# Kernel optimization log

Hardware: AMD Instinct MI355X
Metric: run time of the kernel (lower is better)

The kernel has to match this reference:

```python
import jax, jax.numpy as jnp
import numpy as np

D_INNER = 512; D_STATE = 16; DT_RANK = 32; D_CONV = 4; NUM_NODES = 32
B_ = 4; T_ = 128; F_IN = 64; F_OUT = 64


def setup_inputs() -> dict:
    key = jax.random.key(0)
    ks = jax.random.split(key, 8)
    s = 0.02
    x = jax.random.normal(ks[0], (B_, NUM_NODES, T_, F_IN), jnp.float32)
    adj_matrix = jax.random.randint(ks[1], (NUM_NODES, NUM_NODES), 0, 2, jnp.int32)
    W_in = jax.random.normal(ks[2], (F_IN, 2 * D_INNER), jnp.float32) * s
    W_conv = jax.random.normal(ks[3], (D_INNER, 1, D_CONV), jnp.float32) * s  # depthwise (O,I/g,K)
    b_conv = jnp.zeros((D_INNER,), jnp.float32)
    W_xproj = jax.random.normal(ks[4], (D_INNER, DT_RANK + 2 * D_STATE), jnp.float32) * s
    W_dt = jax.random.normal(ks[5], (DT_RANK, D_INNER), jnp.float32) * s
    b_dt = jnp.zeros((D_INNER,), jnp.float32)
    A_log = jnp.log(jnp.broadcast_to(jnp.arange(1, D_STATE + 1, dtype=jnp.float32), (D_INNER, D_STATE)))
    D = jnp.ones((D_INNER,), jnp.float32)
    W_out = jax.random.normal(ks[6], (D_INNER, F_OUT), jnp.float32) * s
    return dict(x=x, adj_matrix=adj_matrix, W_in=W_in, W_conv=W_conv, b_conv=b_conv,
                W_xproj=W_xproj, W_dt=W_dt, b_dt=b_dt, A_log=A_log, D=D, W_out=W_out)


def reference(x, adj_matrix, W_in, W_conv, b_conv, W_xproj, W_dt, b_dt, A_log, D, W_out):
    b, n_nodes, t, f = x.shape
    u0 = x.reshape(b * n_nodes, t, f)                     # (B, l, f)
    xz = u0 @ W_in                                        # (B, l, 2*d_inner)
    xc, res = jnp.split(xz, 2, axis=-1)
    # causal depthwise conv1d (torch: pad=k-1 both sides then truncate == left-pad k-1)
    xt = jnp.transpose(xc, (0, 2, 1))                     # (B, d, l)
    xt = jnp.pad(xt, ((0, 0), (0, 0), (D_CONV - 1, 0)))
    xt = jax.lax.conv_general_dilated(xt, W_conv, (1,), 'VALID',
        dimension_numbers=('NCH', 'OIH', 'NCH'), feature_group_count=D_INNER)
    xt = xt + b_conv[None, :, None]
    u = jax.nn.silu(jnp.transpose(xt, (0, 2, 1)))         # (B, l, d)
    # SSM parameterization
    A = -jnp.exp(A_log)                                   # (d, n)
    x_dbl = u @ W_xproj
    dlt, Bm, Cm = jnp.split(x_dbl, [DT_RANK, DT_RANK + D_STATE], axis=-1)
    delta = jax.nn.softplus(dlt @ W_dt + b_dt)            # (B, l, d)
    # adjacency padded into ones(d_inner, d_inner) top-left corner
    pad = jnp.ones((D_INNER, D_INNER), jnp.float32)
    pad = pad.at[:NUM_NODES, :NUM_NODES].set(adj_matrix.astype(jnp.float32))
    delta_p = delta @ pad                                 # (B, l, d)
    deltaA = jnp.exp(jnp.einsum('bld,dn->bldn', delta_p, A))
    deltaBu = jnp.einsum('bld,bln->bldn', delta_p * u, Bm)

    def step(h, inp):
        dA_t, dBu_t, C_t = inp
        h = dA_t * h + dBu_t                              # (B, d, n)
        y = jnp.einsum('bdn,bn->bd', h, C_t)
        return h, y

    h0 = jnp.zeros((b * n_nodes, D_INNER, D_STATE), jnp.float32)
    _, ys = jax.lax.scan(step, h0,
        (jnp.moveaxis(deltaA, 1, 0), jnp.moveaxis(deltaBu, 1, 0), jnp.moveaxis(Cm, 1, 0)))
    y = jnp.moveaxis(ys, 0, 1)                            # (B, l, d)
    # original detaches recurrence state and y each step -> scan output carries no grad
    y = jax.lax.stop_gradient(y) + u * D
    y = y * jax.nn.silu(res)
    return y @ W_out                                      # (B, l, dim_out)
```

## Files before the change

### kernel.cpp

```cpp
#include <hip/hip_runtime.h>
#include <cmath>

#define T_    128
#define F_    64
#define DI    512
#define DS    16
#define NROW  16384

#define U_OFF    0u
#define SRES_OFF 8388608u
#define DPH_OFF  16777216u
#define DPT_OFF  17301504u
#define B_OFF    17317888u
#define C_OFF    17580032u

__device__ __forceinline__ float silu_f(float v)    { return v / (1.f + __expf(-v)); }
__device__ __forceinline__ float softplus_f(float v){ return (v > 20.f) ? v : log1pf(__expf(v)); }

__global__ __launch_bounds__(256) void k1_inproj(
    const float* __restrict__ x, const float* __restrict__ W_in,
    const float* __restrict__ W_conv, const float* __restrict__ b_conv,
    float* __restrict__ u, float* __restrict__ sres)
{
    __shared__ float x_l[19][64];
    const int s  = blockIdx.y;
    const int t0 = blockIdx.x * 16;
    const int c4 = threadIdx.x * 4;

    for (int i = threadIdx.x; i < 19 * 16; i += 256) {
        const int row = i >> 4, col = (i & 15) * 4;
        const int trow = t0 - 3 + row;
        float4 v = make_float4(0.f, 0.f, 0.f, 0.f);
        if (trow >= 0) v = *(const float4*)&x[(size_t)s * (T_ * F_) + trow * F_ + col];
        *(float4*)&x_l[row][col] = v;
    }
    __syncthreads();

    float4 acc[19];
#pragma unroll
    for (int i = 0; i < 19; ++i) acc[i] = make_float4(0.f, 0.f, 0.f, 0.f);

    for (int f0 = 0; f0 < F_; f0 += 8) {
        float4 wv[8];
#pragma unroll
        for (int j = 0; j < 8; ++j)
            wv[j] = *(const float4*)&W_in[(size_t)(f0 + j) * 1024 + c4];
#pragma unroll
        for (int tt = 0; tt < 19; ++tt) {
            const float4 xa = *(const float4*)&x_l[tt][f0];
            const float4 xb = *(const float4*)&x_l[tt][f0 + 4];
            float4 a = acc[tt];
            a.x = fmaf(xa.x, wv[0].x, a.x); a.y = fmaf(xa.x, wv[0].y, a.y);
            a.z = fmaf(xa.x, wv[0].z, a.z); a.w = fmaf(xa.x, wv[0].w, a.w);
            a.x = fmaf(xa.y, wv[1].x, a.x); a.y = fmaf(xa.y, wv[1].y, a.y);
            a.z = fmaf(xa.y, wv[1].z, a.z); a.w = fmaf(xa.y, wv[1].w, a.w);
            a.x = fmaf(xa.z, wv[2].x, a.x); a.y = fmaf(xa.z, wv[2].y, a.y);
            a.z = fmaf(xa.z, wv[2].z, a.z); a.w = fmaf(xa.z, wv[2].w, a.w);
            a.x = fmaf(xa.w, wv[3].x, a.x); a.y = fmaf(xa.w, wv[3].y, a.y);
            a.z = fmaf(xa.w, wv[3].z, a.z); a.w = fmaf(xa.w, wv[3].w, a.w);
            a.x = fmaf(xb.x, wv[4].x, a.x); a.y = fmaf(xb.x, wv[4].y, a.y);
            a.z = fmaf(xb.x, wv[4].z, a.z); a.w = fmaf(xb.x, wv[4].w, a.w);
            a.x = fmaf(xb.y, wv[5].x, a.x); a.y = fmaf(xb.y, wv[5].y, a.y);
            a.z = fmaf(xb.y, wv[5].z, a.z); a.w = fmaf(xb.y, wv[5].w, a.w);
            a.x = fmaf(xb.z, wv[6].x, a.x); a.y = fmaf(xb.z, wv[6].y, a.y);
            a.z = fmaf(xb.z, wv[6].z, a.z); a.w = fmaf(xb.z, wv[6].w, a.w);
            a.x = fmaf(xb.w, wv[7].x, a.x); a.y = fmaf(xb.w, wv[7].y, a.y);
            a.z = fmaf(xb.w, wv[7].z, a.z); a.w = fmaf(xb.w, wv[7].w, a.w);
            acc[tt] = a;
        }
    }

    if (c4 < DI) {
        const float4 wk0 = *(const float4*)&W_conv[(c4 + 0) * 4];
        const float4 wk1 = *(const float4*)&W_conv[(c4 + 1) * 4];
        const float4 wk2 = *(const float4*)&W_conv[(c4 + 2) * 4];
        const float4 wk3 = *(const float4*)&W_conv[(c4 + 3) * 4];
        const float4 bc  = *(const float4*)&b_conv[c4];
#pragma unroll
        for (int i = 0; i < 16; ++i) {
            float4 pre;
            pre.x = bc.x; pre.y = bc.y; pre.z = bc.z; pre.w = bc.w;
            pre.x = fmaf(wk0.x, acc[i].x, pre.x); pre.x = fmaf(wk0.y, acc[i+1].x, pre.x);
            pre.x = fmaf(wk0.z, acc[i+2].x, pre.x); pre.x = fmaf(wk0.w, acc[i+3].x, pre.x);
            pre.y = fmaf(wk1.x, acc[i].y, pre.y); pre.y = fmaf(wk1.y, acc[i+1].y, pre.y);
            pre.y = fmaf(wk1.z, acc[i+2].y, pre.y); pre.y = fmaf(wk1.w, acc[i+3].y, pre.y);
            pre.z = fmaf(wk2.x, acc[i].z, pre.z); pre.z = fmaf(wk2.y, acc[i+1].z, pre.z);
            pre.z = fmaf(wk2.z, acc[i+2].z, pre.z); pre.z = fmaf(wk2.w, acc[i+3].z, pre.z);
            pre.w = fmaf(wk3.x, acc[i].w, pre.w); pre.w = fmaf(wk3.y, acc[i+1].w, pre.w);
            pre.w = fmaf(wk3.z, acc[i+2].w, pre.w); pre.w = fmaf(wk3.w, acc[i+3].w, pre.w);
            float4 o;
            o.x = silu_f(pre.x); o.y = silu_f(pre.y);
            o.z = silu_f(pre.z); o.w = silu_f(pre.w);
            *(float4*)&u[(size_t)(s * T_ + t0 + i) * DI + c4] = o;
        }
    } else {
        const int c = c4 - DI;
#pragma unroll
        for (int i = 0; i < 16; ++i) {
            float4 o;
            o.x = silu_f(acc[i + 3].x); o.y = silu_f(acc[i + 3].y);
            o.z = silu_f(acc[i + 3].z); o.w = silu_f(acc[i + 3].w);
            *(float4*)&sres[(size_t)(s * T_ + t0 + i) * DI + c] = o;
        }
    }
}

__global__ __launch_bounds__(256) void k2a_xproj(
    const float* __restrict__ uin, const float* __restrict__ W_xp,
    float* __restrict__ dlt, float* __restrict__ Bb, float* __restrict__ Cb)
{
    __shared__ float y_l[64][68];
    __shared__ float w_l[64][64];
    const int tid = threadIdx.x;
    const int rq = tid >> 4, cq = tid & 15;
    const int r0 = blockIdx.x * 64;
    const int c4 = cq * 4;

    float4 acc[4];
#pragma unroll
    for (int i = 0; i < 4; ++i) acc[i] = make_float4(0.f, 0.f, 0.f, 0.f);

    for (int kc = 0; kc < DI; kc += 64) {
        for (int i = tid; i < 64 * 16; i += 256) {
            const int row = i >> 4, cc = (i & 15) * 4;
            *(float4*)&y_l[row][cc] = *(const float4*)&uin[(size_t)(r0 + row) * DI + kc + cc];
            *(float4*)&w_l[row][cc] = *(const float4*)&W_xp[(size_t)(kc + row) * 64 + cc];
        }
        __syncthreads();
#pragma unroll 4
        for (int kk = 0; kk < 64; kk += 4) {
            float4 yv[4], wv[4];
#pragma unroll
            for (int i = 0; i < 4; ++i) yv[i] = *(const float4*)&y_l[rq * 4 + i][kk];
#pragma unroll
            for (int j = 0; j < 4; ++j) wv[j] = *(const float4*)&w_l[kk + j][c4];
#pragma unroll
            for (int i = 0; i < 4; ++i) {
                float4 a = acc[i];
                a.x = fmaf(yv[i].x, wv[0].x, a.x); a.y = fmaf(yv[i].x, wv[0].y, a.y);
                a.z = fmaf(yv[i].x, wv[0].z, a.z); a.w = fmaf(yv[i].x, wv[0].w, a.w);
                a.x = fmaf(yv[i].y, wv[1].x, a.x); a.y = fmaf(yv[i].y, wv[1].y, a.y);
                a.z = fmaf(yv[i].y, wv[1].z, a.z); a.w = fmaf(yv[i].y, wv[1].w, a.w);
                a.x = fmaf(yv[i].z, wv[2].x, a.x); a.y = fmaf(yv[i].z, wv[2].y, a.y);
                a.z = fmaf(yv[i].z, wv[2].z, a.z); a.w = fmaf(yv[i].z, wv[2].w, a.w);
                a.x = fmaf(yv[i].w, wv[3].x, a.x); a.y = fmaf(yv[i].w, wv[3].y, a.y);
                a.z = fmaf(yv[i].w, wv[3].z, a.z); a.w = fmaf(yv[i].w, wv[3].w, a.w);
                acc[i] = a;
            }
        }
        __syncthreads();
    }
#pragma unroll
    for (int i = 0; i < 4; ++i) {
        const int r = r0 + rq * 4 + i;
        if (c4 < 32)      *(float4*)&dlt[(size_t)r * 32 + c4]        = acc[i];
        else if (c4 < 48) *(float4*)&Bb [(size_t)r * DS + (c4 - 32)] = acc[i];
        else              *(float4*)&Cb [(size_t)r * DS + (c4 - 48)] = acc[i];
    }
}

__global__ __launch_bounds__(256) void k2b_delta(
    const float* __restrict__ dlt_in, const float* __restrict__ W_dt,
    const float* __restrict__ b_dt, const int* __restrict__ adj,
    float* __restrict__ dph, float* __restrict__ dpt)
{
    __shared__ float dl_l[32][32];
    __shared__ float head_l[32][33];
    __shared__ float scrS[4][32];
    __shared__ float stail_l[32];
    __shared__ float adj_l[1024];

    const int tid  = threadIdx.x;
    const int lane = tid & 63, wv4 = tid >> 6;
    const int r0   = blockIdx.x * 32;

    {
        const int row = tid >> 3, cc = (tid & 7) * 4;
        *(float4*)&dl_l[row][cc] = *(const float4*)&dlt_in[(size_t)(r0 + row) * 32 + cc];
        for (int i = tid; i < 1024; i += 256) adj_l[i] = (float)adj[i];
    }

    float wdt0[32], wdt1[32];
#pragma unroll
    for (int j = 0; j < 32; ++j) {
        wdt0[j] = W_dt[j * DI + tid];
        wdt1[j] = W_dt[j * DI + tid + 256];
    }
    const float b0 = b_dt[tid], b1 = b_dt[tid + 256];
    __syncthreads();

    for (int r = 0; r < 32; ++r) {
        float a0 = b0, a1 = b1;
#pragma unroll
        for (int jq = 0; jq < 8; ++jq) {
            const float4 dv = *(const float4*)&dl_l[r][jq * 4];
            a0 = fmaf(dv.x, wdt0[jq*4+0], a0); a1 = fmaf(dv.x, wdt1[jq*4+0], a1);
            a0 = fmaf(dv.y, wdt0[jq*4+1], a0); a1 = fmaf(dv.y, wdt1[jq*4+1], a1);
            a0 = fmaf(dv.z, wdt0[jq*4+2], a0); a1 = fmaf(dv.z, wdt1[jq*4+2], a1);
            a0 = fmaf(dv.w, wdt0[jq*4+3], a0); a1 = fmaf(dv.w, wdt1[jq*4+3], a1);
        }
        const float e0 = softplus_f(a0), e1 = softplus_f(a1);
        if (tid < 32) head_l[r][tid] = e0;
        float v = e0 + e1;
#pragma unroll
        for (int off = 32; off > 0; off >>= 1) v += __shfl_down(v, off, 64);
        if (lane == 0) scrS[wv4][r] = v;
    }
    __syncthreads();
    if (tid < 32) {
        const int r = tid;
        const float st = scrS[0][r] + scrS[1][r] + scrS[2][r] + scrS[3][r];
        dpt[r0 + r] = st;
        float sh = 0.f;
#pragma unroll
        for (int j = 0; j < 32; ++j) sh += head_l[r][j];
        stail_l[r] = st - sh;
    }
    __syncthreads();
#pragma unroll
    for (int k = 0; k < 4; ++k) {
        const int o = k * 256 + tid;
        const int r = o >> 5, dd = o & 31;
        float a = stail_l[r];
#pragma unroll
        for (int j = 0; j < 32; ++j) a = fmaf(head_l[r][j], adj_l[j * 32 + dd], a);
        dph[(size_t)(r0 + r) * 32 + dd] = a;
    }
}

__global__ __launch_bounds__(256) void k3_scan(
    const float* __restrict__ u, float* __restrict__ sres_y,
    const float* __restrict__ dph, const float* __restrict__ dpt,
    const float* __restrict__ Bb, const float* __restrict__ Cb,
    const float* __restrict__ A_log, const float* __restrict__ Dvec)
{
    const int s = blockIdx.y;
    const int d = blockIdx.x * 256 + threadIdx.x;
    float A[DS];
#pragma unroll
    for (int n = 0; n < DS; ++n) A[n] = -__expf(A_log[d * DS + n]);
    const float Dd = Dvec[d];
    const bool isHead = (d < 32);

    const size_t rb = (size_t)s * T_;
    const float* up   = u      + rb * DI + d;
    float*       gp   = sres_y + rb * DI + d;
    const float* dphp = dph + rb * 32 + d;
    const float* dptp = dpt + rb;
    const float4* Bp  = (const float4*)(Bb + rb * DS);
    const float4* Cp  = (const float4*)(Cb + rb * DS);

    float h[DS];
#pragma unroll
    for (int n = 0; n < DS; ++n) h[n] = 0.f;

    float ub[4], gb[4], dpb[4];
#pragma unroll
    for (int j = 0; j < 4; ++j) {
        ub[j]  = up[(size_t)j * DI];
        gb[j]  = gp[(size_t)j * DI];
        dpb[j] = isHead ? dphp[(size_t)j * 32] : dptp[j];
    }
    float4 bB[2][4], bC[2][4];
#pragma unroll
    for (int j = 0; j < 2; ++j)
#pragma unroll
        for (int q = 0; q < 4; ++q) { bB[j][q] = Bp[j * 4 + q]; bC[j][q] = Cp[j * 4 + q]; }

    for (int t = 0; t < T_; t += 4) {
#pragma unroll
        for (int j = 0; j < 4; ++j) {
            const int tc = t + j;
            const float u_c = ub[j], g_c = gb[j], dp_c = dpb[j];
            const float du = dp_c * u_c;
            float y0 = 0.f, y1 = 0.f, y2 = 0.f, y3 = 0.f;
#pragma unroll
            for (int q = 0; q < 4; ++q) {
                const float4 Bv = bB[j & 1][q];
                const float4 Cv = bC[j & 1][q];
                const int n = q * 4;
                const float e0 = __expf(dp_c * A[n + 0]);
                const float e1 = __expf(dp_c * A[n + 1]);
                const float e2 = __expf(dp_c * A[n + 2]);
                const float e3 = __expf(dp_c * A[n + 3]);
                h[n + 0] = fmaf(e0, h[n + 0], du * Bv.x);
                h[n + 1] = fmaf(e1, h[n + 1], du * Bv.y);
                h[n + 2] = fmaf(e2, h[n + 2], du * Bv.z);
                h[n + 3] = fmaf(e3, h[n + 3], du * Bv.w);
                y0 = fmaf(h[n + 0], Cv.x, y0);
                y1 = fmaf(h[n + 1], Cv.y, y1);
                y2 = fmaf(h[n + 2], Cv.z, y2);
                y3 = fmaf(h[n + 3], Cv.w, y3);
            }
            const float yf = (((y0 + y1) + (y2 + y3)) + u_c * Dd) * g_c;
            gp[(size_t)tc * DI] = yf;
            if (tc + 4 < T_) {
                ub[j]  = up[(size_t)(tc + 4) * DI];
                gb[j]  = gp[(size_t)(tc + 4) * DI];
                dpb[j] = isHead ? dphp[(size_t)(tc + 4) * 32] : dptp[tc + 4];
            }
            if (tc + 2 < T_) {
#pragma unroll
                for (int q = 0; q < 4; ++q) {
                    bB[j & 1][q] = Bp[(tc + 2) * 4 + q];
                    bC[j & 1][q] = Cp[(tc + 2) * 4 + q];
                }
            }
        }
    }
}

__global__ __launch_bounds__(256) void k4_out(
    const float* __restrict__ y, const float* __restrict__ W_out,
    float* __restrict__ out)
{
    __shared__ float y_l[64][68];
    __shared__ float w_l[64][64];
    const int tid = threadIdx.x;
    const int rq = tid >> 4, cq = tid & 15;
    const int r0 = blockIdx.x * 64;
    const int c4 = cq * 4;

    float4 acc[4];
#pragma unroll
    for (int i = 0; i < 4; ++i) acc[i] = make_float4(0.f, 0.f, 0.f, 0.f);

    for (int kc = 0; kc < DI; kc += 64) {
        for (int i = tid; i < 64 * 16; i += 256) {
            const int row = i >> 4, cc = (i & 15) * 4;
            *(float4*)&y_l[row][cc] = *(const float4*)&y[(size_t)(r0 + row) * DI + kc + cc];
            *(float4*)&w_l[row][cc] = *(const float4*)&W_out[(size_t)(kc + row) * 64 + cc];
        }
        __syncthreads();
#pragma unroll 4
        for (int kk = 0; kk < 64; kk += 4) {
            float4 yv[4], wv[4];
#pragma unroll
            for (int i = 0; i < 4; ++i) yv[i] = *(const float4*)&y_l[rq * 4 + i][kk];
#pragma unroll
            for (int j = 0; j < 4; ++j) wv[j] = *(const float4*)&w_l[kk + j][c4];
#pragma unroll
            for (int i = 0; i < 4; ++i) {
                float4 a = acc[i];
                a.x = fmaf(yv[i].x, wv[0].x, a.x); a.y = fmaf(yv[i].x, wv[0].y, a.y);
                a.z = fmaf(yv[i].x, wv[0].z, a.z); a.w = fmaf(yv[i].x, wv[0].w, a.w);
                a.x = fmaf(yv[i].y, wv[1].x, a.x); a.y = fmaf(yv[i].y, wv[1].y, a.y);
                a.z = fmaf(yv[i].y, wv[1].z, a.z); a.w = fmaf(yv[i].y, wv[1].w, a.w);
                a.x = fmaf(yv[i].z, wv[2].x, a.x); a.y = fmaf(yv[i].z, wv[2].y, a.y);
                a.z = fmaf(yv[i].z, wv[2].z, a.z); a.w = fmaf(yv[i].z, wv[2].w, a.w);
                a.x = fmaf(yv[i].w, wv[3].x, a.x); a.y = fmaf(yv[i].w, wv[3].y, a.y);
                a.z = fmaf(yv[i].w, wv[3].z, a.z); a.w = fmaf(yv[i].w, wv[3].w, a.w);
                acc[i] = a;
            }
        }
        __syncthreads();
    }
#pragma unroll
    for (int i = 0; i < 4; ++i)
        *(float4*)&out[(size_t)(r0 + rq * 4 + i) * 64 + c4] = acc[i];
}

extern "C" void kernel_launch(void* const* d_in, const int* in_sizes, int n_in,
                              void* d_out, int out_size, void* d_ws, size_t ws_size,
                              hipStream_t stream)
{
    const float* x      = (const float*)d_in[0];
    const int*   adj    = (const int*)  d_in[1];
    const float* W_in   = (const float*)d_in[2];
    const float* W_conv = (const float*)d_in[3];
    const float* b_conv = (const float*)d_in[4];
    const float* W_xp   = (const float*)d_in[5];
    const float* W_dt   = (const float*)d_in[6];
    const float* b_dt   = (const float*)d_in[7];
    const float* A_log  = (const float*)d_in[8];
    const float* Dvec   = (const float*)d_in[9];
    const float* W_out  = (const float*)d_in[10];

    float* ws   = (float*)d_ws;
    float* u    = ws + U_OFF;
    float* sres = ws + SRES_OFF;
    float* dB   = ws + DPH_OFF;
    float* dpt  = ws + DPT_OFF;
    float* Bb   = ws + B_OFF;
    float* Cb   = ws + C_OFF;
    float* out  = (float*)d_out;

    k1_inproj<<<dim3(8, 128), 256, 0, stream>>>(x, W_in, W_conv, b_conv, u, sres);
    k2a_xproj<<<dim3(256),    256, 0, stream>>>(u, W_xp, dB, Bb, Cb);
    k2b_delta<<<dim3(512),    256, 0, stream>>>(dB, W_dt, b_dt, adj, dB, dpt);
    k3_scan  <<<dim3(2, 128), 256, 0, stream>>>(u, sres, dB, dpt, Bb, Cb, A_log, Dvec);
    k4_out   <<<dim3(256),    256, 0, stream>>>(sres, W_out, out);
}
```

Measured before the change: 323.9 us.

## Chunk scan prefetch into 16-step double buffers and halve GEMM row tiles

The scan kernel now prefetches u, gate and delta in 16-timestep chunks into double-buffered register arrays and buffers its outputs per chunk. B and C are loaded directly each step instead of from a small register ring. This aims to hide global-load latency in the serial recurrence and relies on launch_bounds(256,1) to allow the larger register footprint. Separately, the x-projection and output GEMM kernels use 32-row tiles with 128 threads and twice as many blocks, so the 256 CUs get more parallelism, at the cost of loading the shared weight tile more times.

```diff
diff --git a/kernel.cpp b/kernel.cpp
--- a/kernel.cpp
+++ b/kernel.cpp
@@ -105,15 +105,15 @@
     }
 }
 
-__global__ __launch_bounds__(256) void k2a_xproj(
+__global__ __launch_bounds__(128) void k2a_xproj(
     const float* __restrict__ uin, const float* __restrict__ W_xp,
     float* __restrict__ dlt, float* __restrict__ Bb, float* __restrict__ Cb)
 {
-    __shared__ float y_l[64][68];
+    __shared__ float y_l[32][68];
     __shared__ float w_l[64][64];
     const int tid = threadIdx.x;
     const int rq = tid >> 4, cq = tid & 15;
-    const int r0 = blockIdx.x * 64;
+    const int r0 = blockIdx.x * 32;
     const int c4 = cq * 4;
 
     float4 acc[4];
@@ -121,9 +121,12 @@
     for (int i = 0; i < 4; ++i) acc[i] = make_float4(0.f, 0.f, 0.f, 0.f);
 
     for (int kc = 0; kc < DI; kc += 64) {
-        for (int i = tid; i < 64 * 16; i += 256) {
+        for (int i = tid; i < 32 * 16; i += 128) {
             const int row = i >> 4, cc = (i & 15) * 4;
             *(float4*)&y_l[row][cc] = *(const float4*)&uin[(size_t)(r0 + row) * DI + kc + cc];
+        }
+        for (int i = tid; i < 64 * 16; i += 128) {
+            const int row = i >> 4, cc = (i & 15) * 4;
             *(float4*)&w_l[row][cc] = *(const float4*)&W_xp[(size_t)(kc + row) * 64 + cc];
         }
         __syncthreads();
@@ -228,7 +231,54 @@
     }
 }
 
-__global__ __launch_bounds__(256) void k3_scan(
+__device__ __forceinline__ void scan_chunk(
+    int t0, bool pref, int t0n,
+    const float* __restrict__ up, float* __restrict__ gp,
+    const float* __restrict__ dp_ptr, int dstr,
+    const float4* __restrict__ Bp, const float4* __restrict__ Cp,
+    const float (&A)[DS], float Dd, float (&h)[DS],
+    float (&ucur)[16], float (&gcur)[16], float (&dcur)[16],
+    float (&unxt)[16], float (&gnxt)[16], float (&dnxt)[16])
+{
+    if (pref) {
+#pragma unroll
+        for (int j = 0; j < 16; ++j) {
+            unxt[j] = up[(size_t)(t0n + j) * DI];
+            gnxt[j] = gp[(size_t)(t0n + j) * DI];
+            dnxt[j] = dp_ptr[(t0n + j) * dstr];
+        }
+    }
+    float yf[16];
+#pragma unroll
+    for (int j = 0; j < 16; ++j) {
+        const float u_c = ucur[j], g_c = gcur[j], dp_c = dcur[j];
+        const float du = dp_c * u_c;
+        float y0 = 0.f, y1 = 0.f, y2 = 0.f, y3 = 0.f;
+#pragma unroll
+        for (int q = 0; q < 4; ++q) {
+            const float4 Bv = Bp[(t0 + j) * 4 + q];
+            const float4 Cv = Cp[(t0 + j) * 4 + q];
+            const int n = q * 4;
+            const float e0 = __expf(dp_c * A[n + 0]);
+            const float e1 = __expf(dp_c * A[n + 1]);
+            const float e2 = __expf(dp_c * A[n + 2]);
+            const float e3 = __expf(dp_c * A[n + 3]);
+            h[n + 0] = fmaf(e0, h[n + 0], du * Bv.x);
+            h[n + 1] = fmaf(e1, h[n + 1], du * Bv.y);
+            h[n + 2] = fmaf(e2, h[n + 2], du * Bv.z);
+            h[n + 3] = fmaf(e3, h[n + 3], du * Bv.w);
+            y0 = fmaf(h[n + 0], Cv.x, y0);
+            y1 = fmaf(h[n + 1], Cv.y, y1);
+            y2 = fmaf(h[n + 2], Cv.z, y2);
+            y3 = fmaf(h[n + 3], Cv.w, y3);
+        }
+        yf[j] = (((y0 + y1) + (y2 + y3)) + u_c * Dd) * g_c;
+    }
+#pragma unroll
+    for (int j = 0; j < 16; ++j) gp[(size_t)(t0 + j) * DI] = yf[j];
+}
+
+__global__ __launch_bounds__(256, 1) void k3_scan(
     const float* __restrict__ u, float* __restrict__ sres_y,
     const float* __restrict__ dph, const float* __restrict__ dpt,
     const float* __restrict__ Bb, const float* __restrict__ Cb,
@@ -243,82 +293,42 @@
     const bool isHead = (d < 32);
 
     const size_t rb = (size_t)s * T_;
-    const float* up   = u      + rb * DI + d;
-    float*       gp   = sres_y + rb * DI + d;
-    const float* dphp = dph + rb * 32 + d;
-    const float* dptp = dpt + rb;
-    const float4* Bp  = (const float4*)(Bb + rb * DS);
-    const float4* Cp  = (const float4*)(Cb + rb * DS);
+    const float* up = u + rb * DI + d;
+    float*       gp = sres_y + rb * DI + d;
+    const float* dp_ptr = isHead ? (dph + rb * 32 + d) : (dpt + rb);
+    const int dstr = isHead ? 32 : 1;
+    const float4* Bp = (const float4*)(Bb + rb * DS);
+    const float4* Cp = (const float4*)(Cb + rb * DS);
 
     float h[DS];
 #pragma unroll
     for (int n = 0; n < DS; ++n) h[n] = 0.f;
 
-    float ub[4], gb[4], dpb[4];
-#pragma unroll
-    for (int j = 0; j < 4; ++j) {
-        ub[j]  = up[(size_t)j * DI];
-        gb[j]  = gp[(size_t)j * DI];
-        dpb[j] = isHead ? dphp[(size_t)j * 32] : dptp[j];
-    }
-    float4 bB[2][4], bC[2][4];
-#pragma unroll
-    for (int j = 0; j < 2; ++j)
-#pragma unroll
-        for (int q = 0; q < 4; ++q) { bB[j][q] = Bp[j * 4 + q]; bC[j][q] = Cp[j * 4 + q]; }
-
-    for (int t = 0; t < T_; t += 4) {
-#pragma unroll
-        for (int j = 0; j < 4; ++j) {
-            const int tc = t + j;
-            const float u_c = ub[j], g_c = gb[j], dp_c = dpb[j];
-            const float du = dp_c * u_c;
-            float y0 = 0.f, y1 = 0.f, y2 = 0.f, y3 = 0.f;
-#pragma unroll
-            for (int q = 0; q < 4; ++q) {
-                const float4 Bv = bB[j & 1][q];
-                const float4 Cv = bC[j & 1][q];
-                const int n = q * 4;
-                const float e0 = __expf(dp_c * A[n + 0]);
-                const float e1 = __expf(dp_c * A[n + 1]);
-                const float e2 = __expf(dp_c * A[n + 2]);
-                const float e3 = __expf(dp_c * A[n + 3]);
-                h[n + 0] = fmaf(e0, h[n + 0], du * Bv.x);
-                h[n + 1] = fmaf(e1, h[n + 1], du * Bv.y);
-                h[n + 2] = fmaf(e2, h[n + 2], du * Bv.z);
-                h[n + 3] = fmaf(e3, h[n + 3], du * Bv.w);
-                y0 = fmaf(h[n + 0], Cv.x, y0);
-                y1 = fmaf(h[n + 1], Cv.y, y1);
-                y2 = fmaf(h[n + 2], Cv.z, y2);
-                y3 = fmaf(h[n + 3], Cv.w, y3);
-            }
-            const float yf = (((y0 + y1) + (y2 + y3)) + u_c * Dd) * g_c;
-            gp[(size_t)tc * DI] = yf;
-            if (tc + 4 < T_) {
-                ub[j]  = up[(size_t)(tc + 4) * DI];
-                gb[j]  = gp[(size_t)(tc + 4) * DI];
-                dpb[j] = isHead ? dphp[(size_t)(tc + 4) * 32] : dptp[tc + 4];
-            }
-            if (tc + 2 < T_) {
-#pragma unroll
-                for (int q = 0; q < 4; ++q) {
-                    bB[j & 1][q] = Bp[(tc + 2) * 4 + q];
-                    bC[j & 1][q] = Cp[(tc + 2) * 4 + q];
-                }
-            }
-        }
-    }
-}
-
-__global__ __launch_bounds__(256) void k4_out(
+    float uA[16], gA[16], dA_[16], uB[16], gB[16], dB_[16];
+#pragma unroll
+    for (int j = 0; j < 16; ++j) {
+        uA[j]  = up[(size_t)j * DI];
+        gA[j]  = gp[(size_t)j * DI];
+        dA_[j] = dp_ptr[j * dstr];
+    }
+
+    for (int c = 0; c < 8; c += 2) {
+        scan_chunk(c * 16, true, (c + 1) * 16, up, gp, dp_ptr, dstr, Bp, Cp,
+                   A, Dd, h, uA, gA, dA_, uB, gB, dB_);
+        scan_chunk((c + 1) * 16, c + 2 < 8, (c + 2) * 16, up, gp, dp_ptr, dstr, Bp, Cp,
+                   A, Dd, h, uB, gB, dB_, uA, gA, dA_);
+    }
+}
+
+__global__ __launch_bounds__(128) void k4_out(
     const float* __restrict__ y, const float* __restrict__ W_out,
     float* __restrict__ out)
 {
-    __shared__ float y_l[64][68];
+    __shared__ float y_l[32][68];
     __shared__ float w_l[64][64];
     const int tid = threadIdx.x;
     const int rq = tid >> 4, cq = tid & 15;
-    const int r0 = blockIdx.x * 64;
+    const int r0 = blockIdx.x * 32;
     const int c4 = cq * 4;
 
     float4 acc[4];
@@ -326,9 +336,12 @@
     for (int i = 0; i < 4; ++i) acc[i] = make_float4(0.f, 0.f, 0.f, 0.f);
 
     for (int kc = 0; kc < DI; kc += 64) {
-        for (int i = tid; i < 64 * 16; i += 256) {
+        for (int i = tid; i < 32 * 16; i += 128) {
             const int row = i >> 4, cc = (i & 15) * 4;
             *(float4*)&y_l[row][cc] = *(const float4*)&y[(size_t)(r0 + row) * DI + kc + cc];
+        }
+        for (int i = tid; i < 64 * 16; i += 128) {
+            const int row = i >> 4, cc = (i & 15) * 4;
             *(float4*)&w_l[row][cc] = *(const float4*)&W_out[(size_t)(kc + row) * 64 + cc];
         }
         __syncthreads();
@@ -386,8 +399,8 @@
     float* out  = (float*)d_out;
 
     k1_inproj<<<dim3(8, 128), 256, 0, stream>>>(x, W_in, W_conv, b_conv, u, sres);
-    k2a_xproj<<<dim3(256),    256, 0, stream>>>(u, W_xp, dB, Bb, Cb);
+    k2a_xproj<<<dim3(512),    128, 0, stream>>>(u, W_xp, dB, Bb, Cb);
     k2b_delta<<<dim3(512),    256, 0, stream>>>(dB, W_dt, b_dt, adj, dB, dpt);
     k3_scan  <<<dim3(2, 128), 256, 0, stream>>>(u, sres, dB, dpt, Bb, Cb, A_log, Dvec);
-    k4_out   <<<dim3(256),    256, 0, stream>>>(sres, W_out, out);
-}
+    k4_out   <<<dim3(512),    128, 0, stream>>>(sres, W_out, out);
+}
```

After: 338.5 us. 4.5% more time.
